# Performance work log

Hardware: AMD Instinct MI355X
Metric: run time of the kernel (lower is better)

Reference implementation:

```python
import jax, jax.numpy as jnp
import numpy as np

B, S, HID = 4, 2048, 1024
NH = 16
HD = HID // NH  # 64


def setup_inputs() -> dict:
    key = jax.random.key(0)
    k1, k2, k3 = jax.random.split(key, 3)
    x = jax.random.normal(k1, (B, S, HID), dtype=jnp.float32)
    # causal sparse mask: True = attend
    mask = jnp.tril(jnp.ones((S, S), dtype=bool))
    w_qkv = jax.random.normal(k2, (HID, 3 * HID), dtype=jnp.float32) * 0.02
    b_qkv = jnp.zeros((3 * HID,), dtype=jnp.float32)
    w_out = jax.random.normal(k3, (HID, HID), dtype=jnp.float32) * 0.02
    b_out = jnp.zeros((HID,), dtype=jnp.float32)
    return {"x": x, "mask": mask, "w_qkv": w_qkv, "b_qkv": b_qkv,
            "w_out": w_out, "b_out": b_out}


def reference(x, mask, w_qkv, b_qkv, w_out, b_out):
    bsz, seq_len, hid = x.shape
    # QKV projection -> [B, S, H, 3*D] -> [B, H, S, 3*D]
    qkv = (x @ w_qkv + b_qkv).reshape(bsz, seq_len, NH, 3 * HD).transpose(0, 2, 1, 3)
    q, k, v = jnp.split(qkv, 3, axis=-1)  # each [B, H, S, D]
    scale = 1.0 / jnp.sqrt(jnp.asarray(HD, dtype=x.dtype))
    scores = jnp.einsum('bhqd,bhkd->bhqk', q, k) * scale
    scores = jnp.where(mask[None, None, :, :], scores, jnp.asarray(-jnp.inf, dtype=scores.dtype))
    probs = jax.nn.softmax(scores, axis=-1)
    context = jnp.einsum('bhqk,bhkd->bhqd', probs, v)  # [B, H, S, D]
    context = context.transpose(0, 2, 1, 3).reshape(bsz, seq_len, hid)
    return context @ w_out + b_out
```

## Files before the change

### kernel.cpp

```cpp
#include <hip/hip_runtime.h>
#include <stdint.h>

#define S_LEN 2048
#define NHEAD 16
#define HDIM  64
#define HIDDEN 1024
#define BATCH 4

typedef float f32x4 __attribute__((ext_vector_type(4)));
typedef __bf16 bf16x8 __attribute__((ext_vector_type(8)));
typedef unsigned short u16;

union U4B8 { uint4 u; bf16x8 b; };

__device__ __forceinline__ bf16x8 as_b8(uint4 u){ U4B8 x; x.u = u; return x.b; }

__device__ __forceinline__ f32x4 mfma16(uint4 a, uint4 b, f32x4 c){
  return __builtin_amdgcn_mfma_f32_16x16x32_bf16(as_b8(a), as_b8(b), c, 0, 0, 0);
}

__device__ __forceinline__ u16 f2bf(float f){
  __bf16 h = (__bf16)f;
  return __builtin_bit_cast(u16, h);
}

__device__ __forceinline__ float exp2fast(float x){
  return __builtin_exp2f(x);
}

__device__ __forceinline__ void gload16(const void* g, void* l){
  __builtin_amdgcn_global_load_lds(
      (const __attribute__((address_space(1))) unsigned int*)g,
      (__attribute__((address_space(3))) unsigned int*)l, 16, 0, 0);
}

#define QSCALE 0.18033688f
#define DEFER_THR 11.5f

__global__ __launch_bounds__(256) void k_cvt(const float* __restrict__ in,
                                             u16* __restrict__ out, int n4){
  int i = blockIdx.x * 256 + threadIdx.x;
  int stride = gridDim.x * 256;
  for (; i < n4; i += stride){
    float4 v = ((const float4*)in)[i];
    unsigned lo = (unsigned)f2bf(v.x) | ((unsigned)f2bf(v.y) << 16);
    unsigned hi = (unsigned)f2bf(v.z) | ((unsigned)f2bf(v.w) << 16);
    ((uint2*)out)[i] = make_uint2(lo, hi);
  }
}

__global__ __launch_bounds__(256) void k_transpose(const float* __restrict__ in,
                                                   u16* __restrict__ out,
                                                   int K, int N){
  __shared__ float t[32][33];
  int tx = threadIdx.x & 31, ty = threadIdx.x >> 5;
  int n0 = blockIdx.x * 32, k0 = blockIdx.y * 32;
  #pragma unroll
  for (int i = 0; i < 4; ++i)
    t[ty + i*8][tx] = in[(size_t)(k0 + ty + i*8) * N + n0 + tx];
  __syncthreads();
  #pragma unroll
  for (int i = 0; i < 4; ++i)
    out[(size_t)(n0 + ty + i*8) * K + k0 + tx] = f2bf(t[tx][ty + i*8]);
}

template<int MODE>
__global__ __launch_bounds__(256) void k_gemm(
    const u16* __restrict__ A, const u16* __restrict__ Bt,
    const float* __restrict__ bias,
    u16* __restrict__ oq, u16* __restrict__ ok, u16* __restrict__ ov,
    float* __restrict__ of, int M, int N, int K)
{
  __shared__ u16 As[128 * 32];
  __shared__ u16 Bs[128 * 32];
  const int tid  = threadIdx.x;
  const int wave = tid >> 6, lane = tid & 63;
  const int l4 = lane >> 4, lm = lane & 15;
  const int wr = wave >> 1, wc = wave & 1;
  const int row0 = blockIdx.y * 128;
  const int col0 = blockIdx.x * 128;

  const f32x4 fzero = {0.f, 0.f, 0.f, 0.f};
  f32x4 acc[4][4];
  #pragma unroll
  for (int m = 0; m < 4; ++m)
    #pragma unroll
    for (int n = 0; n < 4; ++n) acc[m][n] = fzero;

  for (int k0 = 0; k0 < K; k0 += 32){
    #pragma unroll
    for (int p = 0; p < 2; ++p){
      int chunk = wave * 128 + p * 64 + lane;
      int r = chunk >> 2, cseg = chunk & 3;
      const u16* ga = A  + (size_t)(row0 + r) * K + k0 + cseg * 8;
      gload16(ga, &As[(wave * 128 + p * 64) * 8]);
      const u16* gb = Bt + (size_t)(col0 + r) * K + k0 + cseg * 8;
      gload16(gb, &Bs[(wave * 128 + p * 64) * 8]);
    }
    __syncthreads();
    uint4 af[4], bf[4];
    #pragma unroll
    for (int m = 0; m < 4; ++m)
      af[m] = *(const uint4*)&As[(wr * 64 + m * 16 + lm) * 32 + l4 * 8];
    #pragma unroll
    for (int n = 0; n < 4; ++n)
      bf[n] = *(const uint4*)&Bs[(wc * 64 + n * 16 + lm) * 32 + l4 * 8];
    #pragma unroll
    for (int m = 0; m < 4; ++m)
      #pragma unroll
      for (int n = 0; n < 4; ++n)
        acc[m][n] = mfma16(af[m], bf[n], acc[m][n]);
    __syncthreads();
  }

  #pragma unroll
  for (int m = 0; m < 4; ++m){
    #pragma unroll
    for (int n = 0; n < 4; ++n){
      int c = col0 + wc * 64 + n * 16 + lm;
      float bv = bias[c];
      #pragma unroll
      for (int r = 0; r < 4; ++r){
        int row = row0 + wr * 64 + m * 16 + l4 * 4 + r;
        float val = acc[m][n][r] + bv;
        if (MODE == 0){
          int h = c / 192, e = c % 192;
          int which = e >> 6, d = e & 63;
          int b = row >> 11, s = row & 2047;
          int bh = b * 16 + h;
          if (which == 2){
            ov[((size_t)bh * HDIM + d) * S_LEN + s] = f2bf(val);
          } else {
            if (which == 0) val *= QSCALE;
            size_t idx = ((size_t)bh * S_LEN + s) * HDIM + d;
            u16* dst = (which == 0) ? oq : ok;
            dst[idx] = f2bf(val);
          }
        } else {
          of[(size_t)row * N + c] = val;
        }
      }
    }
  }
}

__device__ __forceinline__ void stage_tile(
    const u16* __restrict__ kB, const u16* __restrict__ vB,
    u16* ldsK, u16* ldsV, int kbase, int wave, int lane)
{
  #pragma unroll
  for (int p = 0; p < 2; ++p){
    int ch  = wave * 128 + p * 64 + lane;
    int row = ch >> 3;
    int cc  = (ch & 7) << 4;
    int sc  = cc ^ ((row & 7) << 4);
    const u16* gk = kB + (size_t)(kbase + row) * HDIM + (sc >> 1);
    gload16(gk, ldsK + (size_t)(wave * 128 + p * 64) * 8);
    const u16* gv = vB + (size_t)row * S_LEN + kbase + (sc >> 1);
    gload16(gv, ldsV + (size_t)(wave * 128 + p * 64) * 8);
  }
}

__global__ __launch_bounds__(256) void k_attn(
    const u16* __restrict__ q, const u16* __restrict__ kk,
    const u16* __restrict__ vt, u16* __restrict__ ctx)
{
  __shared__ u16 KV[2][2][64 * 64];
  __shared__ u16 Ps[4][2][16][72];

  const int bid = blockIdx.x;
  const int bh = bid & 63;
  const int pr = bid >> 6;
  const int wave = threadIdx.x >> 6, lane = threadIdx.x & 63;
  const int l4 = lane >> 4, lm = lane & 15;
  const size_t base = (size_t)bh * (S_LEN * HDIM);
  const u16* kB = kk + base;
  const u16* vB = vt + base;
  const int b = bh >> 4, h = bh & 15;
  const f32x4 fz = {0.f, 0.f, 0.f, 0.f};

  #pragma unroll 1
  for (int half = 0; half < 2; ++half){
    const int st = half ? (15 - pr) : pr;
    const int q0 = st * 128 + wave * 32;

    uint4 qf[2][2];
    #pragma unroll
    for (int f = 0; f < 2; ++f){
      const u16* qr = q + base + (size_t)(q0 + f * 16 + lm) * HDIM + l4 * 8;
      qf[f][0] = *(const uint4*)qr;
      qf[f][1] = *(const uint4*)(qr + 32);
    }

    float mr[2] = {-1e30f, -1e30f}, lsp[2] = {0.f, 0.f};
    f32x4 acc[2][4];
    #pragma unroll
    for (int f = 0; f < 2; ++f)
      #pragma unroll
      for (int tt = 0; tt < 4; ++tt) acc[f][tt] = fz;

    const int nkt = 2 * st + 2;

    stage_tile(kB, vB, &KV[0][0][0], &KV[0][1][0], 0, wave, lane);

    #pragma unroll 1
    for (int kt = 0; kt < nkt; ++kt){
      const int cur = kt & 1;
      const int kbase = kt << 6;
      if (kt + 1 < nkt){
        stage_tile(kB, vB, &KV[cur ^ 1][0][0], &KV[cur ^ 1][1][0],
                   (kt + 1) << 6, wave, lane);
        asm volatile("s_waitcnt vmcnt(4)" ::: "memory");
      } else {
        asm volatile("s_waitcnt vmcnt(0)" ::: "memory");
      }
      __builtin_amdgcn_s_barrier();
      asm volatile("" ::: "memory");

      if (kbase < q0 + 32){
        const u16* ldsK = &KV[cur][0][0];
        const u16* ldsV = &KV[cur][1][0];

        f32x4 sv[2][4];
        __builtin_amdgcn_s_setprio(1);
        #pragma unroll
        for (int g = 0; g < 4; ++g){
          int rk = g * 16 + lm;
          int xa = (l4 * 16) ^ ((rk & 7) << 4);
          int xb = (64 + l4 * 16) ^ ((rk & 7) << 4);
          const u16* krow = ldsK + rk * 64;
          uint4 kf0 = *(const uint4*)(krow + (xa >> 1));
          uint4 kf1 = *(const uint4*)(krow + (xb >> 1));
          sv[0][g] = mfma16(kf0, qf[0][0], fz);
          sv[0][g] = mfma16(kf1, qf[0][1], sv[0][g]);
          sv[1][g] = mfma16(kf0, qf[1][0], fz);
          sv[1][g] = mfma16(kf1, qf[1][1], sv[1][g]);
        }
        __builtin_amdgcn_s_setprio(0);

        const bool tail = (kbase + 63 > q0);

        #pragma unroll
        for (int f = 0; f < 2; ++f){
          if (tail){
            #pragma unroll
            for (int g = 0; g < 4; ++g)
              #pragma unroll
              for (int r = 0; r < 4; ++r){
                int kg = kbase + g * 16 + l4 * 4 + r;
                int qg = q0 + f * 16 + lm;
                if (kg > qg) sv[f][g][r] = -1e30f;
              }
          }

          float pm = sv[f][0][0];
          #pragma unroll
          for (int g = 0; g < 4; ++g)
            #pragma unroll
            for (int r = 0; r < 4; ++r) pm = fmaxf(pm, sv[f][g][r]);
          pm = fmaxf(pm, __shfl_xor(pm, 16));
          pm = fmaxf(pm, __shfl_xor(pm, 32));

          if (__any(pm > mr[f] + DEFER_THR)){
            float mn = fmaxf(mr[f], pm);
            float corr = exp2fast(mr[f] - mn);
            mr[f] = mn;
            lsp[f] *= corr;
            float cf[4];
            #pragma unroll
            for (int r = 0; r < 4; ++r) cf[r] = __shfl(corr, l4 * 4 + r);
            #pragma unroll
            for (int tt = 0; tt < 4; ++tt)
              #pragma unroll
              for (int r = 0; r < 4; ++r) acc[f][tt][r] *= cf[r];
          }

          float s_ = 0.f;
          #pragma unroll
          for (int g = 0; g < 4; ++g){
            float p0 = exp2fast(sv[f][g][0] - mr[f]);
            float p1 = exp2fast(sv[f][g][1] - mr[f]);
            float p2 = exp2fast(sv[f][g][2] - mr[f]);
            float p3 = exp2fast(sv[f][g][3] - mr[f]);
            s_ += (p0 + p1) + (p2 + p3);
            uint2 w;
            w.x = (unsigned)f2bf(p0) | ((unsigned)f2bf(p1) << 16);
            w.y = (unsigned)f2bf(p2) | ((unsigned)f2bf(p3) << 16);
            *(uint2*)&Ps[wave][f][lm][g * 16 + l4 * 4] = w;
          }
          lsp[f] += s_;
        }

        __builtin_amdgcn_wave_barrier();
        uint4 pa[2][2];
        #pragma unroll
        for (int f = 0; f < 2; ++f){
          pa[f][0] = *(const uint4*)&Ps[wave][f][lm][l4 * 8];
          pa[f][1] = *(const uint4*)&Ps[wave][f][lm][32 + l4 * 8];
        }

        __builtin_amdgcn_s_setprio(1);
        #pragma unroll
        for (int tt = 0; tt < 4; ++tt){
          int rv = tt * 16 + lm;
          int xa = (l4 * 16) ^ ((rv & 7) << 4);
          int xb = (64 + l4 * 16) ^ ((rv & 7) << 4);
          const u16* vrow = ldsV + rv * 64;
          uint4 v0 = *(const uint4*)(vrow + (xa >> 1));
          uint4 v1 = *(const uint4*)(vrow + (xb >> 1));
          acc[0][tt] = mfma16(pa[0][0], v0, acc[0][tt]);
          acc[0][tt] = mfma16(pa[0][1], v1, acc[0][tt]);
          acc[1][tt] = mfma16(pa[1][0], v0, acc[1][tt]);
          acc[1][tt] = mfma16(pa[1][1], v1, acc[1][tt]);
        }
        __builtin_amdgcn_s_setprio(0);
      }

      asm volatile("" ::: "memory");
      __builtin_amdgcn_s_barrier();
      asm volatile("" ::: "memory");
    }

    #pragma unroll
    for (int f = 0; f < 2; ++f){
      lsp[f] += __shfl_xor(lsp[f], 16);
      lsp[f] += __shfl_xor(lsp[f], 32);
      float inv_ = 1.0f / lsp[f];
      float ivr[4];
      #pragma unroll
      for (int r = 0; r < 4; ++r) ivr[r] = __shfl(inv_, l4 * 4 + r);
      #pragma unroll
      for (int tt = 0; tt < 4; ++tt)
        #pragma unroll
        for (int r = 0; r < 4; ++r){
          int srow = q0 + f * 16 + l4 * 4 + r;
          float val = acc[f][tt][r] * ivr[r];
          ctx[((size_t)b * S_LEN + srow) * HIDDEN + h * HDIM + tt * 16 + lm] = f2bf(val);
        }
    }
  }
}

extern "C" void kernel_launch(void* const* d_in, const int* in_sizes, int n_in,
                              void* d_out, int out_size, void* d_ws, size_t ws_size,
                              hipStream_t stream)
{
  const float* x     = (const float*)d_in[0];
  const float* w_qkv = (const float*)d_in[2];
  const float* b_qkv = (const float*)d_in[3];
  const float* w_out = (const float*)d_in[4];
  const float* b_out = (const float*)d_in[5];

  char* ws = (char*)d_ws;
  u16* xbf   = (u16*)(ws);
  u16* wqkvT = (u16*)(ws + 16777216);
  u16* woutT = (u16*)(ws + 23068672);
  u16* qb    = (u16*)(ws + 25165824);
  u16* kb    = (u16*)(ws + 41943040);
  u16* vb    = (u16*)(ws + 58720256);

  k_cvt<<<2048, 256, 0, stream>>>(x, xbf, (BATCH * S_LEN * HIDDEN) / 4);
  k_transpose<<<dim3(96, 32), 256, 0, stream>>>(w_qkv, wqkvT, HIDDEN, 3 * HIDDEN);
  k_transpose<<<dim3(32, 32), 256, 0, stream>>>(w_out, woutT, HIDDEN, HIDDEN);
  k_gemm<0><<<dim3(24, 64), 256, 0, stream>>>(xbf, wqkvT, b_qkv,
                                              qb, kb, vb, nullptr,
                                              BATCH * S_LEN, 3 * HIDDEN, HIDDEN);
  k_attn<<<512, 256, 0, stream>>>(qb, kb, vb, xbf);
  k_gemm<1><<<dim3(8, 64), 256, 0, stream>>>(xbf, woutT, b_out,
                                             nullptr, nullptr, nullptr,
                                             (float*)d_out, BATCH * S_LEN, HIDDEN, HIDDEN);
}
```

Before: 228.0 us.

## Double-buffer GEMM LDS tiles with async prefetch and MFMA priority

```diff
diff --git a/kernel.cpp b/kernel.cpp
--- a/kernel.cpp
+++ b/kernel.cpp
@@ -64,6 +64,21 @@
     out[(size_t)(n0 + ty + i*8) * K + k0 + tx] = f2bf(t[tx][ty + i*8]);
 }
 
+__device__ __forceinline__ void stage_gemm(
+    const u16* __restrict__ A, const u16* __restrict__ Bt,
+    u16* As, u16* Bs, int row0, int col0, int K, int k0, int wave, int lane)
+{
+  #pragma unroll
+  for (int p = 0; p < 2; ++p){
+    int chunk = wave * 128 + p * 64 + lane;
+    int r = chunk >> 2, cseg = chunk & 3;
+    const u16* ga = A  + (size_t)(row0 + r) * K + k0 + cseg * 8;
+    gload16(ga, As + (size_t)(wave * 128 + p * 64) * 8);
+    const u16* gb = Bt + (size_t)(col0 + r) * K + k0 + cseg * 8;
+    gload16(gb, Bs + (size_t)(wave * 128 + p * 64) * 8);
+  }
+}
+
 template<int MODE>
 __global__ __launch_bounds__(256) void k_gemm(
     const u16* __restrict__ A, const u16* __restrict__ Bt,
@@ -71,8 +86,8 @@
     u16* __restrict__ oq, u16* __restrict__ ok, u16* __restrict__ ov,
     float* __restrict__ of, int M, int N, int K)
 {
-  __shared__ u16 As[128 * 32];
-  __shared__ u16 Bs[128 * 32];
+  __shared__ u16 As[2][128 * 32];
+  __shared__ u16 Bs[2][128 * 32];
   const int tid  = threadIdx.x;
   const int wave = tid >> 6, lane = tid & 63;
   const int l4 = lane >> 4, lm = lane & 15;
@@ -87,30 +102,40 @@
     #pragma unroll
     for (int n = 0; n < 4; ++n) acc[m][n] = fzero;
 
-  for (int k0 = 0; k0 < K; k0 += 32){
-    #pragma unroll
-    for (int p = 0; p < 2; ++p){
-      int chunk = wave * 128 + p * 64 + lane;
-      int r = chunk >> 2, cseg = chunk & 3;
-      const u16* ga = A  + (size_t)(row0 + r) * K + k0 + cseg * 8;
-      gload16(ga, &As[(wave * 128 + p * 64) * 8]);
-      const u16* gb = Bt + (size_t)(col0 + r) * K + k0 + cseg * 8;
-      gload16(gb, &Bs[(wave * 128 + p * 64) * 8]);
-    }
-    __syncthreads();
+  stage_gemm(A, Bt, &As[0][0], &Bs[0][0], row0, col0, K, 0, wave, lane);
+
+  const int nks = K >> 5;
+  #pragma unroll 1
+  for (int ks = 0; ks < nks; ++ks){
+    const int cur = ks & 1;
+    if (ks + 1 < nks){
+      stage_gemm(A, Bt, &As[cur ^ 1][0], &Bs[cur ^ 1][0],
+                 row0, col0, K, (ks + 1) << 5, wave, lane);
+      asm volatile("s_waitcnt vmcnt(4)" ::: "memory");
+    } else {
+      asm volatile("s_waitcnt vmcnt(0)" ::: "memory");
+    }
+    __builtin_amdgcn_s_barrier();
+    asm volatile("" ::: "memory");
+
     uint4 af[4], bf[4];
     #pragma unroll
     for (int m = 0; m < 4; ++m)
-      af[m] = *(const uint4*)&As[(wr * 64 + m * 16 + lm) * 32 + l4 * 8];
+      af[m] = *(const uint4*)&As[cur][(wr * 64 + m * 16 + lm) * 32 + l4 * 8];
     #pragma unroll
     for (int n = 0; n < 4; ++n)
-      bf[n] = *(const uint4*)&Bs[(wc * 64 + n * 16 + lm) * 32 + l4 * 8];
+      bf[n] = *(const uint4*)&Bs[cur][(wc * 64 + n * 16 + lm) * 32 + l4 * 8];
+    __builtin_amdgcn_s_setprio(1);
     #pragma unroll
     for (int m = 0; m < 4; ++m)
       #pragma unroll
       for (int n = 0; n < 4; ++n)
         acc[m][n] = mfma16(af[m], bf[n], acc[m][n]);
-    __syncthreads();
+    __builtin_amdgcn_s_setprio(0);
+
+    asm volatile("" ::: "memory");
+    __builtin_amdgcn_s_barrier();
+    asm volatile("" ::: "memory");
   }
 
   #pragma unroll
```

Result: faster. 218.3 us (-4.3%).
